# Kernel optimization log

Hardware: AMD Instinct MI355X
Metric: run time of the kernel (lower is better)

## Reference

```python
import jax, jax.numpy as jnp
import numpy as np

TUCKER_RANKS = (8, 2, 6, 2)
N_ITER = 5  # fixed HOOI (ALS) sweeps; tensorly.tucker uses tol-based early stop with n_iter_max=100


def _unfold(t, n):
    return jnp.moveaxis(t, n, 0).reshape(t.shape[n], -1)


def _top_left_vecs(X, r):
    # top-r left singular vectors of X, via eigh on the smaller Gram matrix
    d, k = X.shape
    if d <= k:
        _, v = jnp.linalg.eigh(X @ X.T)  # ascending eigvals
        return v[:, ::-1][:, :r]
    w, v = jnp.linalg.eigh(X.T @ X)
    w = w[::-1][:r]
    v = v[:, ::-1][:, :r]
    return (X @ v) / jnp.sqrt(jnp.maximum(w, 1e-12))


def _mode_dot_t(t, U, mode):
    # tensor x_mode U^T : contracts dim `mode` (size d) down to U.shape[1] (rank r)
    return jnp.moveaxis(jnp.tensordot(t, U, axes=([mode], [0])), -1, mode)


def _project(t, factors, skip):
    # contract modes with the biggest reduction first so intermediates stay tiny
    order = sorted((m for m in range(t.ndim) if m != skip),
                   key=lambda m: factors[m].shape[1] / t.shape[m])
    y = t
    for m in order:
        y = _mode_dot_t(y, factors[m], m)
    return y


def _tucker(t, ranks, n_iter):
    # HOSVD init + HOOI (ALS) sweeps, as in tensorly.decomposition.tucker
    factors = [_top_left_vecs(_unfold(t, n), r) for n, r in enumerate(ranks)]
    for _ in range(n_iter):
        for n in range(len(ranks)):
            y = _project(t, factors, skip=n)
            factors[n] = _top_left_vecs(_unfold(y, n), ranks[n])
    core = _project(t, factors, skip=-1)
    return core, factors


def _forward(state, action, conv_w, conv_b, wa, ba, wq, bq):
    sv = jax.lax.conv_general_dilated(
        state[None], conv_w, window_strides=(1, 1, 1), padding='VALID',
        dimension_numbers=('NCDHW', 'OIDHW', 'NCDHW'))[0]
    sv = jax.nn.relu(sv + conv_b[:, None, None, None])   # [32, 96, 384, 24]
    core, _ = _tucker(sv, TUCKER_RANKS, N_ITER)           # [8, 2, 6, 2]
    av = jax.nn.relu(action @ wa.T + ba)                  # [192]
    sav = jax.nn.relu(core.reshape(-1) + av)              # [192]
    return sav @ wq.T + bq                                # [1]


def setup_inputs() -> dict:
    key = jax.random.key(0)
    ks = jax.random.split(key, 8)
    n_actions = 96
    core_dim = 8 * 2 * 6 * 2  # 192
    return {
        'state': jax.random.normal(ks[0], (4, 96, 386, 24), dtype=jnp.float32),
        'action': jax.random.uniform(ks[1], (n_actions,), dtype=jnp.float32),
        'conv_w': jax.random.normal(ks[2], (32, 4, 1, 3, 1), dtype=jnp.float32) * 0.1,
        'conv_b': jax.random.normal(ks[3], (32,), dtype=jnp.float32) * 0.1,
        'wa': jax.random.normal(ks[4], (core_dim, n_actions), dtype=jnp.float32) * 0.1,
        'ba': jax.random.normal(ks[5], (core_dim,), dtype=jnp.float32) * 0.1,
        'wq': jax.random.normal(ks[6], (1, core_dim), dtype=jnp.float32) * 0.1,
        'bq': jax.random.normal(ks[7], (1,), dtype=jnp.float32) * 0.1,
    }


def reference(state, action, conv_w, conv_b, wa, ba, wq, bq):
    return _forward(state, action, conv_w, conv_b, wa, ba, wq, bq)
```

## Files before the change

kernel.cpp:

```cpp
#include <hip/hip_runtime.h>
#include <math.h>

#define TPB 256
#define SMLSIZ 25
#define D_EPS    1.1102230246251565e-16
#define D_SAFMIN 2.2250738585072014e-308
#define CMDMAX 8192
#define SCHUNK 64

__device__ __forceinline__ double d_sign(double a, double b){
  double aa = fabs(a);
  return (b >= 0.0) ? aa : -aa;
}
__device__ __forceinline__ double dlapy2(double x, double y){
  double xa = fabs(x), ya = fabs(y);
  double w = fmax(xa, ya), z = fmin(xa, ya);
  if (z == 0.0) return w;
  double t = z / w;
  return w * sqrt(1.0 + t*t);
}
__device__ void dlartg(double f, double g, double* cs, double* sn, double* r){
  if (g == 0.0) { *cs = 1.0; *sn = 0.0; *r = f; return; }
  if (f == 0.0) { *cs = 0.0; *sn = (g >= 0.0) ? 1.0 : -1.0; *r = fabs(g); return; }
  double f1 = fabs(f), g1 = fabs(g);
  double rtmin = sqrt(D_SAFMIN);
  double rtmax = sqrt(1.0/(2.0*D_SAFMIN));
  if (f1 > rtmin && f1 < rtmax && g1 > rtmin && g1 < rtmax) {
    double d = sqrt(f*f + g*g);
    *cs = f1 / d;
    double rr = (f >= 0.0) ? d : -d;
    *sn = g / rr;
    *r = rr;
  } else {
    double safmax = 1.0/D_SAFMIN;
    double u = fmin(safmax, fmax(fmax(D_SAFMIN, f1), g1));
    double fs = f/u, gs = g/u;
    double d = sqrt(fs*fs + gs*gs);
    *cs = fabs(fs)/d;
    double rr = (f >= 0.0) ? d : -d;
    *sn = gs / rr;
    *r = rr * u;
  }
}
__device__ void dlaev2(double a, double b, double c,
                       double* rt1, double* rt2, double* cs1, double* sn1){
  double sm = a + c, df = a - c, adf = fabs(df), tb = b + b, ab = fabs(tb);
  double acmx, acmn;
  if (fabs(a) > fabs(c)) { acmx = a; acmn = c; } else { acmx = c; acmn = a; }
  double rt;
  if (adf > ab)      { double t = ab/adf; rt = adf*sqrt(1.0+t*t); }
  else if (adf < ab) { double t = adf/ab; rt = ab*sqrt(1.0+t*t); }
  else               rt = ab*sqrt(2.0);
  int sgn1;
  if (sm < 0.0)      { *rt1 = 0.5*(sm-rt); sgn1 = -1; *rt2 = (acmx / *rt1)*acmn - (b / *rt1)*b; }
  else if (sm > 0.0) { *rt1 = 0.5*(sm+rt); sgn1 =  1; *rt2 = (acmx / *rt1)*acmn - (b / *rt1)*b; }
  else               { *rt1 = 0.5*rt; *rt2 = -0.5*rt; sgn1 = 1; }
  int sgn2; double cs;
  if (df >= 0.0) { cs = df + rt; sgn2 = 1; } else { cs = df - rt; sgn2 = -1; }
  double acs = fabs(cs);
  if (acs > ab) {
    double ct = -tb/cs;
    *sn1 = 1.0/sqrt(1.0+ct*ct);
    *cs1 = ct * (*sn1);
  } else {
    if (ab == 0.0) { *cs1 = 1.0; *sn1 = 0.0; }
    else { double tn = -cs/tb; *cs1 = 1.0/sqrt(1.0+tn*tn); *sn1 = tn * (*cs1); }
  }
  if (sgn1 == sgn2) { double tn = *cs1; *cs1 = -(*sn1); *sn1 = tn; }
}
__device__ void dlamrg(int n1, int n2, const double* a, int s1, int s2, int* idx){
  int n1sv = n1, n2sv = n2;
  int ind1 = (s1 > 0) ? 0 : n1-1;
  int ind2 = (s2 > 0) ? n1 : n1+n2-1;
  int i = 0;
  while (n1sv > 0 && n2sv > 0) {
    if (a[ind1] <= a[ind2]) { idx[i++] = ind1; ind1 += s1; n1sv--; }
    else                    { idx[i++] = ind2; ind2 += s2; n2sv--; }
  }
  while (n1sv > 0) { idx[i++] = ind1; ind1 += s1; n1sv--; }
  while (n2sv > 0) { idx[i++] = ind2; ind2 += s2; n2sv--; }
}

__device__ void my_laed5(int i, const double* d, const double* z, double rho,
                         double* delta, double* lam){
  double del = d[1]-d[0];
  if (i == 0) {
    double w = 1.0 + 2.0*rho*(z[1]*z[1]-z[0]*z[0])/del;
    if (w > 0.0) {
      double b = del + rho*(z[0]*z[0]+z[1]*z[1]);
      double c = rho*z[0]*z[0]*del;
      double tau = 2.0*c/(b+sqrt(fabs(b*b-4.0*c)));
      *lam = d[0] + tau;
      delta[0] = -z[0]/tau;
      delta[1] =  z[1]/(del-tau);
    } else {
      double b = -del + rho*(z[0]*z[0]+z[1]*z[1]);
      double c = rho*z[1]*z[1]*del;
      double tau;
      if (b > 0.0) tau = -2.0*c/(b+sqrt(b*b+4.0*c));
      else         tau = (b - sqrt(b*b+4.0*c))/2.0;
      *lam = d[1] + tau;
      delta[0] = -z[0]/(del+tau);
      delta[1] = -z[1]/tau;
    }
    double temp = dlapy2(delta[0], delta[1]);
    delta[0] /= temp; delta[1] /= temp;
  } else {
    double b = -del + rho*(z[0]*z[0]+z[1]*z[1]);
    double c = rho*z[1]*z[1]*del;
    double tau;
    if (b > 0.0) tau = (b+sqrt(b*b+4.0*c))/2.0;
    else         tau = 2.0*c/(-b+sqrt(b*b+4.0*c));
    *lam = d[1] + tau;
    delta[0] = -z[0]/(del+tau);
    delta[1] = -z[1]/tau;
    double temp = dlapy2(delta[0], delta[1]);
    delta[0] /= temp; delta[1] /= temp;
  }
}
__device__ void my_laed4(int k, int j, const double* dl, const double* w, double rho,
                         double* delta, double* lam){
  if (k == 1) { *lam = dl[0] + rho*w[0]*w[0]; delta[0] = 1.0; return; }
  if (k == 2) { my_laed5(j, dl, w, rho, delta, lam); return; }
  int base; double a, b;
  if (j < k-1) {
    double dj = dl[j], dj1 = dl[j+1];
    double mid = 0.5*(dj+dj1);
    double fm = 1.0;
#pragma unroll 4
    for (int i = 0; i < k; i++) fm += rho*w[i]*w[i]/(dl[i]-mid);
    if (fm >= 0.0) { base = j;   a = 0.0;      b = mid - dj;  }
    else           { base = j+1; a = mid - dj1; b = 0.0;      }
  } else {
    base = k-1;
    double zz = 0.0;
#pragma unroll 4
    for (int i = 0; i < k; i++) zz += w[i]*w[i];
    a = 0.0; b = rho*zz;
    for (int t = 0; t < 64; t++) {
      double g = 1.0;
#pragma unroll 4
      for (int i = 0; i < k; i++) g += rho*w[i]*w[i]/((dl[i]-dl[base]) - b);
      if (g >= 0.0) break;
      b *= 2.0;
    }
  }
  for (int it = 0; it < 140; it++) {
    double m = 0.5*(a+b);
    if (m == a || m == b) break;
    double g = 1.0;
#pragma unroll 4
    for (int i = 0; i < k; i++) g += rho*w[i]*w[i]/((dl[i]-dl[base]) - m);
    if (g >= 0.0) b = m; else a = m;
  }
  double tau = 0.5*(a+b);
  *lam = dl[base] + tau;
#pragma unroll 4
  for (int i = 0; i < k; i++) delta[i] = (dl[i]-dl[base]) - tau;
}

struct Cmd { double c, s; int a, b; };
// ... 590 lines not shown
            }
            __syncthreads();
            if (K == 2) {
              if (tid == 0) {
                for (int j = 0; j < 2; j++) {
                  double a0 = qb[(size_t)j*ldn + 0], a1 = qb[(size_t)j*ldn + 1];
                  qb[(size_t)j*ldn + 0] = (indxc[0] == 0) ? a0 : a1;
                  qb[(size_t)j*ldn + 1] = (indxc[1] == 0) ? a0 : a1;
                }
              }
              __syncthreads();
            } else if (K >= 3) {
              for (int i = tid; i < K; i += NT) szv[i] = sw[i];
              __syncthreads();
              for (int i = tid; i < K; i += NT) {
                double prod = qb[(size_t)i*ldn + i];
#pragma unroll 4
                for (int j = 0; j < K; j++) {
                  if (j == i) continue;
                  prod *= qb[(size_t)j*ldn + i] / (sdl[i]-sdl[j]);
                }
                sw[i] = d_sign(sqrt(fmax(-prod, 0.0)), szv[i]);
              }
              __syncthreads();
              for (int j = tid; j < K; j += NT) {
                double nrm = 0.0;
#pragma unroll 4
                for (int i = 0; i < K; i++) {
                  double v = sw[i]/qb[(size_t)j*ldn + i];
                  sbuf[(size_t)j*K + i] = v;
                  nrm += v*v;
                }
                ss2[j] = sqrt(nrm);
              }
              __syncthreads();
              for (int fl = tid; fl < K*K; fl += NT) {
                int jj2 = fl/K, i = fl%K;
                qb[(size_t)jj2*ldn + i] = sbuf[(size_t)jj2*K + indxc[i]] / ss2[jj2];
              }
              __syncthreads();
            }
            int n12 = ct0+ct1, n23 = ct1+ct2;
            for (int fl = tid; fl < n23*K; fl += NT) {
              int jj2 = fl/n23, i = fl%n23;
              sbuf[(size_t)jj2*n23 + i] = qb[(size_t)jj2*ldn + ct0 + i];
            }
            __syncthreads();
            for (int fl = tid; fl < n2c*K; fl += NT) {
              int jj2 = fl/n2c, r = fl%n2c;
              const double* srow = sbuf + (size_t)jj2*n23;
              double acc = 0.0;
              int l = 0;
              int rem = n23 & 7;
              for (; l < rem; l++) acc += q2[base2 + (size_t)l*n2c + r] * srow[l];
              for (; l < n23; l += 8) {
                double x0 = q2[base2 + (size_t)(l+0)*n2c + r];
                double x1 = q2[base2 + (size_t)(l+1)*n2c + r];
                double x2 = q2[base2 + (size_t)(l+2)*n2c + r];
                double x3 = q2[base2 + (size_t)(l+3)*n2c + r];
                double x4 = q2[base2 + (size_t)(l+4)*n2c + r];
                double x5 = q2[base2 + (size_t)(l+5)*n2c + r];
                double x6 = q2[base2 + (size_t)(l+6)*n2c + r];
                double x7 = q2[base2 + (size_t)(l+7)*n2c + r];
                double y0 = srow[l+0], y1 = srow[l+1], y2 = srow[l+2], y3 = srow[l+3];
                double y4 = srow[l+4], y5 = srow[l+5], y6 = srow[l+6], y7 = srow[l+7];
                acc += x0*y0; acc += x1*y1; acc += x2*y2; acc += x3*y3;
                acc += x4*y4; acc += x5*y5; acc += x6*y6; acc += x7*y7;
              }
              qb[(size_t)jj2*ldn + n1 + r] = acc;
            }
            __syncthreads();
            for (int fl = tid; fl < n12*K; fl += NT) {
              int jj2 = fl/n12, i = fl%n12;
              sbuf[(size_t)jj2*n12 + i] = qb[(size_t)jj2*ldn + i];
            }
            __syncthreads();
            for (int fl = tid; fl < n1*K; fl += NT) {
              int jj2 = fl/n1, r = fl%n1;
              const double* srow = sbuf + (size_t)jj2*n12;
              double acc = 0.0;
              int l = 0;
              int rem = n12 & 7;
              for (; l < rem; l++) acc += q2[(size_t)l*n1 + r] * srow[l];
              for (; l < n12; l += 8) {
                double x0 = q2[(size_t)(l+0)*n1 + r];
                double x1 = q2[(size_t)(l+1)*n1 + r];
                double x2 = q2[(size_t)(l+2)*n1 + r];
                double x3 = q2[(size_t)(l+3)*n1 + r];
                double x4 = q2[(size_t)(l+4)*n1 + r];
                double x5 = q2[(size_t)(l+5)*n1 + r];
                double x6 = q2[(size_t)(l+6)*n1 + r];
                double x7 = q2[(size_t)(l+7)*n1 + r];
                double y0 = srow[l+0], y1 = srow[l+1], y2 = srow[l+2], y3 = srow[l+3];
                double y4 = srow[l+4], y5 = srow[l+5], y6 = srow[l+6], y7 = srow[l+7];
                acc += x0*y0; acc += x1*y1; acc += x2*y2; acc += x3*y3;
                acc += x4*y4; acc += x5*y5; acc += x6*y6; acc += x7*y7;
              }
              qb[(size_t)jj2*ldn + r] = acc;
            }
            __syncthreads();
            if (tid == 0) dlamrg(K, nm-K, dm, 1, -1, ixq);
            __syncthreads();
          }
        }
        if (tid == 0) iw[i2/2] = iw[i2+1];
        __syncthreads();
      }
      sp /= 2;
    }
    {
      int msz2 = finish - startb + 1;
      for (int i = tid; i < msz2; i += NT) dtmp[i] = sd[startb + indxq[startb+i]];
      for (int fl = tid; fl < msz2*msz2; fl += NT) {
        int i = fl/msz2, r = fl%msz2;
        qtmp[(size_t)i*msz2 + r] = Z[(size_t)(startb + indxq[startb+i])*n + startb + r];
      }
      __syncthreads();
      for (int i = tid; i < msz2; i += NT) sd[startb+i] = dtmp[i];
      for (int fl = tid; fl < msz2*msz2; fl += NT) {
        int i = fl/msz2, r = fl%msz2;
        Z[(size_t)(startb+i)*n + startb + r] = qtmp[(size_t)i*msz2 + r];
      }
      __syncthreads();
      if (tid == 0) {
        double onrm = dcom[7];
        for (int i = startb; i <= finish; i++) sd[i] *= onrm;
      }
      __syncthreads();
    }
    startb = finish + 1;
  }
  if (nblk > 1) {
    for (int ii = 1; ii <= n-1; ii++) {
      if (tid == 0) {
        int i = ii-1, kk = i; double p = sd[i];
        for (int j = ii; j <= n-1; j++) if (sd[j] < p) { kk = j; p = sd[j]; }
        icom[7] = kk;
        if (kk != i) { sd[kk] = sd[i]; sd[i] = p; }
      }
      __syncthreads();
      int kk = icom[7], i = ii-1;
      if (kk != i) {
        for (int r = tid; r < n; r += NT) {
          double t = Z[(size_t)i*n + r];
          Z[(size_t)i*n + r] = Z[(size_t)kk*n + r];
          Z[(size_t)kk*n + r] = t;
        }
      }
      __syncthreads();
    }
  }
}

template<int NT, int MAXN>
__global__ __launch_bounds__(NT) void k_eigh_small(int n, const double* __restrict__ Ain,
                                                   double* __restrict__ Zout,
                                                   double* __restrict__ Dout,
                                                   double* gwrk){
  __shared__ double sd[MAXN], se[MAXN], stau[MAXN], sdl[MAXN], sw[MAXN], szv[MAXN], ss2[MAXN];
  __shared__ double red[NT], dcom[8];
  __shared__ int indx[MAXN], indxc[MAXN], indxp[MAXN], coltyp[MAXN], indxq[MAXN];
  __shared__ int iw[40], icom[16], icom2[16];
  __shared__ Cmd scmd[SCHUNK];
  extern __shared__ double dyn[];
  double* A = dyn;
  double* Z = dyn + n*n;
  const int tid = threadIdx.x;

  for (int x = tid; x < n*n; x += NT) A[x] = Ain[x];
  __syncthreads();

  sytd2_dev<NT>(n, A, sd, se, stau, szv, red, dcom);

  for (int x = tid; x < n*n; x += NT) Z[x] = ((x % (n+1)) == 0) ? 1.0 : 0.0;
  __syncthreads();

  stedc_dev<NT>(n, Z, gwrk, sd, se, sdl, sw, szv, ss2, dcom,
                indx, indxc, indxp, coltyp, indxq, iw, icom, icom2, scmd);

  __syncthreads();
  for (int j = tid; j < n; j += NT) {
    for (int ii = n-2; ii >= 0; ii--) {
      double tau_i = stau[ii];
      if (tau_i == 0.0) continue;
      double w = Z[(size_t)j*n + ii + 1];
#pragma unroll 4
      for (int r = ii+2; r < n; r++) w += A[(size_t)ii*n + r] * Z[(size_t)j*n + r];
      w *= tau_i;
      Z[(size_t)j*n + ii + 1] -= w;
#pragma unroll 4
      for (int r = ii+2; r < n; r++) Z[(size_t)j*n + r] -= w * A[(size_t)ii*n + r];
    }
  }
  __syncthreads();
  for (int x = tid; x < n*n; x += NT) Zout[x] = Z[x];
  for (int i = tid; i < n; i += NT) Dout[i] = sd[i];
}

template<int NT>
__global__ __launch_bounds__(NT) void k_sytd2_big(int n, double* A,
                                                  double* gsd, double* gse, double* gtau){
  __shared__ double sd[384], se[384], stau[384], vv[384], ww[384];
  __shared__ double red[16], dcom[8];
  const int tid = threadIdx.x;
  sytd2_big<NT>(n, A, sd, se, stau, vv, ww, red, dcom);
  for (int i = tid; i < n; i += NT) {
    gsd[i] = sd[i];
    gtau[i] = stau[i];
    if (i < n-1) gse[i] = se[i];
  }
}

template<int NT>
__global__ __launch_bounds__(NT) void k_stedc_big(int n, double* Z, double* Dout,
                                                  double* gwrk,
                                                  const double* gsd, const double* gse){
  __shared__ double sd[384], se[384], sdl[384], sw[384], szv[384], ss2[384];
  __shared__ double dcom[8];
  __shared__ int indx[384], indxc[384], indxp[384], coltyp[384], indxq[384];
  __shared__ int iw[40], icom[16], icom2[16];
  __shared__ Cmd scmd[SCHUNK];
  const int tid = threadIdx.x;

  for (int i = tid; i < n; i += NT) {
    sd[i] = gsd[i];
    if (i < n-1) se[i] = gse[i];
  }
  for (size_t x = tid; x < (size_t)n*n; x += NT) Z[x] = ((x % (size_t)(n+1)) == 0) ? 1.0 : 0.0;
  __syncthreads();

  stedc_dev<NT>(n, Z, gwrk, sd, se, sdl, sw, szv, ss2, dcom,
                indx, indxc, indxp, coltyp, indxq, iw, icom, icom2, scmd);

  for (int i = tid; i < n; i += NT) Dout[i] = sd[i];
}

#define OB_COLS 8
__global__ __launch_bounds__(256) void k_ormtr_big(int n, const double* __restrict__ A,
                                                   double* __restrict__ Z,
                                                   const double* __restrict__ tau,
                                                   int col0base){
  __shared__ double zc[OB_COLS][384];
  __shared__ double vsh[384];
  int col0 = col0base + blockIdx.x * OB_COLS;
  int tid = threadIdx.x;
  int c = tid >> 5;
  int l = tid & 31;
  for (int x = tid; x < OB_COLS*n; x += 256) {
    int cc = x / n, r = x % n;
    if (col0+cc < n) zc[cc][r] = Z[(size_t)(col0+cc)*n + r];
  }
  __syncthreads();
  for (int ii = n-2; ii >= 0; ii--) {
    double ti = tau[ii];
    if (ti != 0.0) {
      for (int r = ii+2+tid; r < n; r += 256) vsh[r] = A[(size_t)ii*n + r];
      __syncthreads();
      double p = (l == 0) ? zc[c][ii+1] : 0.0;
#pragma unroll 4
      for (int r = ii+2+l; r < n; r += 32) p += vsh[r]*zc[c][r];
      for (int off = 16; off > 0; off >>= 1) p += __shfl_down(p, off, 32);
      double w = __shfl(p, 0, 32) * ti;
      if (l == 0) zc[c][ii+1] -= w;
#pragma unroll 4
      for (int r = ii+2+l; r < n; r += 32) zc[c][r] -= w*vsh[r];
      __syncthreads();
    }
  }
  for (int x = tid; x < OB_COLS*n; x += 256) {
    int cc = x / n, r = x % n;
    if (col0+cc < n) Z[(size_t)(col0+cc)*n + r] = zc[cc][r];
  }
}

__global__ __launch_bounds__(TPB) void k_conv(const float* __restrict__ st,
                                              const float* __restrict__ cw,
                                              const float* __restrict__ cb,
                                              float* __restrict__ sv){
  int idx = blockIdx.x*TPB + threadIdx.x;
  if (idx >= 28311552) return;
  int w = idx % 24; int t = idx/24;
  int h = t % 384; t /= 384;
  int d = t % 96; int o = t/96;
  float acc = cb[o];
  for (int i = 0; i < 4; i++)
    for (int kh = 0; kh < 3; kh++)
      acc += st[(((size_t)i*96+d)*386 + h+kh)*24 + w] * cw[(o*4+i)*3 + kh];
  sv[idx] = fmaxf(acc, 0.0f);
}

__global__ __launch_bounds__(TPB) void k_g0p(const float* __restrict__ sv, double* parts){
  __shared__ float slab[32*25];
  int b = blockIdx.x;
  double acc[4]; int c1s[4], c2s[4];
#pragma unroll
  for (int k = 0; k < 4; k++) { int e = threadIdx.x + k*TPB; acc[k] = 0.0; c1s[k] = e/32; c2s[k] = e%32; }
  for (int q = 0; q < 128; q++) {
    int s = b*128 + q; int d = s/384, p = s%384;
    for (int l = threadIdx.x; l < 768; l += TPB) {
      int cc = l/24, w = l-cc*24;
      slab[cc*25+w] = sv[(((size_t)cc*96+d)*384+p)*24 + w];
    }
    __syncthreads();
#pragma unroll
    for (int k = 0; k < 4; k++) {
      double sacc = 0.0;
      const float* r1 = slab + c1s[k]*25;
      const float* r2 = slab + c2s[k]*25;
      for (int w = 0; w < 24; w++) sacc += (double)r1[w]*(double)r2[w];
      acc[k] += sacc;
    }
    __syncthreads();
  }
  for (int k = 0; k < 4; k++) parts[(size_t)b*1024 + threadIdx.x + k*TPB] = acc[k];
}
__global__ __launch_bounds__(TPB) void k_g1p(const float* __restrict__ sv, double* parts){
  __shared__ float slab[96*25];
  int c = blockIdx.x;
  double acc[36]; int d1s[36], d2s[36];
#pragma unroll
  for (int k = 0; k < 36; k++) { int e = threadIdx.x + k*TPB; acc[k] = 0.0; d1s[k] = e/96; d2s[k] = e%96; }
  for (int p = 0; p < 384; p++) {
    for (int l = threadIdx.x; l < 2304; l += TPB) {
      int d = l/24, w = l-d*24;
      slab[d*25+w] = sv[(((size_t)c*96+d)*384+p)*24 + w];
    }
    __syncthreads();
#pragma unroll
    for (int k = 0; k < 36; k++) {
      double sacc = 0.0;
      const float* r1 = slab + d1s[k]*25;
      const float* r2 = slab + d2s[k]*25;
      for (int w = 0; w < 24; w++) sacc += (double)r1[w]*(double)r2[w];
      acc[k] += sacc;
    }
    __syncthreads();
  }
  for (int k = 0; k < 36; k++) parts[(size_t)c*9216 + threadIdx.x + k*TPB] = acc[k];
}
#define G2_NKG 6
__global__ __launch_bounds__(TPB) void k_g2p(const float* __restrict__ sv, double* parts){
  __shared__ float aS[64*25], bS[64*25];
  int blk = blockIdx.x;
  int kg = blk/36, t2 = blk%36, tI = t2/6, tJ = t2%6;
  int tr = (threadIdx.x/16)*4, tc = (threadIdx.x%16)*4;
  double acc[4][4];
#pragma unroll
  for (int i = 0; i < 4; i++)
#pragma unroll
    for (int j = 0; j < 4; j++) acc[i][j] = 0.0;
  for (int ss = 0; ss < 512; ss++) {
    int s = kg*512 + ss;
    size_t base = (size_t)s*9216;
    for (int l = threadIdx.x; l < 1536; l += TPB) {
      int row = l/24, w = l-row*24;
      aS[row*25+w] = sv[base + (size_t)tI*1536 + l];
      bS[row*25+w] = sv[base + (size_t)tJ*1536 + l];
    }
    __syncthreads();
    for (int w = 0; w < 24; w++) {
      double a0 = aS[(tr+0)*25+w], a1 = aS[(tr+1)*25+w], a2 = aS[(tr+2)*25+w], a3 = aS[(tr+3)*25+w];
      double b0 = bS[(tc+0)*25+w], b1 = bS[(tc+1)*25+w], b2 = bS[(tc+2)*25+w], b3 = bS[(tc+3)*25+w];
      acc[0][0]+=a0*b0; acc[0][1]+=a0*b1; acc[0][2]+=a0*b2; acc[0][3]+=a0*b3;
      acc[1][0]+=a1*b0; acc[1][1]+=a1*b1; acc[1][2]+=a1*b2; acc[1][3]+=a1*b3;
      acc[2][0]+=a2*b0; acc[2][1]+=a2*b1; acc[2][2]+=a2*b2; acc[2][3]+=a2*b3;
      acc[3][0]+=a3*b0; acc[3][1]+=a3*b1; acc[3][2]+=a3*b2; acc[3][3]+=a3*b3;
    }
    __syncthreads();
  }
  for (int i = 0; i < 4; i++)
    for (int j = 0; j < 4; j++)
      parts[(size_t)kg*147456 + (size_t)(tI*64+tr+i)*384 + (tJ*64+tc+j)] = acc[i][j];
}
__global__ __launch_bounds__(TPB) void k_g3p(const float* __restrict__ sv, double* parts){
  __shared__ float slab[9216];
  int b = blockIdx.x;
  double acc[3]; int w1s[3], w2s[3];
#pragma unroll
  for (int k = 0; k < 3; k++) { int e = threadIdx.x + k*TPB; acc[k] = 0.0; w1s[k] = e/24; w2s[k] = e%24; }
  for (int q = 0; q < 24; q++) {
    int s = b*24 + q;
    size_t base = (size_t)s*9216;
    for (int l = threadIdx.x; l < 9216; l += TPB) slab[l] = sv[base + l];
    __syncthreads();
#pragma unroll
    for (int k = 0; k < 3; k++) {
      int e = threadIdx.x + k*TPB;
// ... 66 lines not shown
    long t = idx;
    int i3 = (int)(t % os3); t /= os3;
    int i2 = (int)(t % os2); t /= os2;
    int i1 = (int)(t % os1); int i0 = (int)(t/os1);
    int j;
    long base; long st; int sa;
    if (ax == 0)      { j = i0; base = (long)i1*str1 + i2*str2 + i3; st = str0; sa = s0; }
    else if (ax == 1) { j = i1; base = (long)i0*str0 + i2*str2 + i3; st = str1; sa = s1; }
    else if (ax == 2) { j = i2; base = (long)i0*str0 + i1*str1 + i3; st = str2; sa = s2; }
    else              { j = i3; base = (long)i0*str0 + i1*str1 + i2*str2; st = str3; sa = s3; }
    double acc = 0.0;
#pragma unroll 4
    for (int c = 0; c < sa; c++) acc += in[base + (long)c*st] * U[c*r + j];
    out[idx] = acc;
  }
}

__global__ __launch_bounds__(TPB) void k_gram_sw0(const double* __restrict__ y, double* G){
  for (int e = threadIdx.x; e < 576; e += TPB) {
    int c1 = e/24, c2 = e%24;
    double acc = 0.0;
#pragma unroll 4
    for (int i = 0; i < 32; i++) acc += y[i*24+c1]*y[i*24+c2];
    G[e] = acc;
  }
}
__global__ __launch_bounds__(TPB) void k_gram_sw1(const double* __restrict__ y, double* G){
  for (int e = threadIdx.x; e < 9216; e += TPB) {
    int d1 = e/96, d2 = e%96;
    double acc = 0.0;
#pragma unroll 2
    for (int a = 0; a < 8; a++)
#pragma unroll
      for (int ee = 0; ee < 6; ee++)
#pragma unroll
        for (int m = 0; m < 2; m++)
          acc += y[(((size_t)a*96+d1)*6+ee)*2+m]*y[(((size_t)a*96+d2)*6+ee)*2+m];
    G[e] = acc;
  }
}
__global__ __launch_bounds__(TPB) void k_gram_sw2(const double* __restrict__ y, double* G){
  for (int e = threadIdx.x; e < 1024; e += TPB) {
    int q1 = e/32, q2 = e%32;
    double acc = 0.0;
#pragma unroll 4
    for (int p = 0; p < 384; p++)
      acc += y[(size_t)(q1>>1)*768 + p*2 + (q1&1)]*y[(size_t)(q2>>1)*768 + p*2 + (q2&1)];
    G[e] = acc;
  }
}
__global__ __launch_bounds__(TPB) void k_gram_sw3(const double* __restrict__ y, double* G){
  for (int e = threadIdx.x; e < 576; e += TPB) {
    int w1 = e/24, w2 = e%24;
    double acc = 0.0;
#pragma unroll 2
    for (int a = 0; a < 8; a++)
#pragma unroll
      for (int j = 0; j < 2; j++)
#pragma unroll
        for (int ee = 0; ee < 6; ee++)
          acc += y[(((size_t)a*2+j)*6+ee)*24+w1]*y[(((size_t)a*2+j)*6+ee)*24+w2];
    G[e] = acc;
  }
}

__global__ __launch_bounds__(TPB) void k_fact_sq(double* U, const double* Z, int n, int r){
  int t = blockIdx.x*TPB + threadIdx.x;
  if (t >= n*r) return;
  int i = t/r, j = t%r;
  U[t] = Z[(size_t)(n-1-j)*n + i];
}
__global__ __launch_bounds__(TPB) void k_factT0(double* U0, const double* y,
                                                const double* Z, const double* D){
  int t = threadIdx.x;
  if (t >= 256) return;
  int i = t/8, j = t%8;
  int col = 23-j;
  double acc = 0.0;
#pragma unroll 4
  for (int c = 0; c < 24; c++) acc += y[i*24+c]*Z[(size_t)col*24+c];
  U0[t] = acc / sqrt(fmax(D[col], 1e-12));
}
__global__ __launch_bounds__(TPB) void k_factT2(double* U2, const double* y,
                                                const double* Z, const double* D){
  int t = blockIdx.x*TPB + threadIdx.x;
  if (t >= 2304) return;
  int p = t/6, j = t%6;
  int col = 31-j;
  double acc = 0.0;
#pragma unroll 4
  for (int q = 0; q < 32; q++)
    acc += y[(size_t)(q>>1)*768 + p*2 + (q&1)]*Z[(size_t)col*32+q];
  U2[t] = acc / sqrt(fmax(D[col], 1e-12));
}

__global__ __launch_bounds__(TPB) void k_tail(const double* __restrict__ core,
                                              const float* __restrict__ action,
                                              const float* __restrict__ wa,
                                              const float* __restrict__ ba,
                                              const float* __restrict__ wq,
                                              const float* __restrict__ bq,
                                              float* __restrict__ out){
  __shared__ double s[TPB];
  int t = threadIdx.x;
  double v = 0.0;
  if (t < 192) {
    double av = 0.0;
#pragma unroll 4
    for (int i = 0; i < 96; i++) av += (double)action[i]*(double)wa[t*96+i];
    av += (double)ba[t];
    if (av < 0.0) av = 0.0;
    double sav = core[t] + av;
    if (sav < 0.0) sav = 0.0;
    v = sav * (double)wq[t];
  }
  s[t] = v; __syncthreads();
  for (int st = 128; st > 0; st >>= 1) { if (t < st) s[t] += s[t+st]; __syncthreads(); }
  if (t == 0) out[0] = (float)(s[0] + (double)bq[0]);
}
__global__ void k_fail(float* out){ out[0] = 1234.5f; }

extern "C" void kernel_launch(void* const* d_in, const int* in_sizes, int n_in,
                              void* d_out, int out_size, void* d_ws, size_t ws_size,
                              hipStream_t stream){
  (void)in_sizes; (void)n_in; (void)out_size;
  const float* state  = (const float*)d_in[0];
  const float* action = (const float*)d_in[1];
  const float* conv_w = (const float*)d_in[2];
  const float* conv_b = (const float*)d_in[3];
  const float* wa     = (const float*)d_in[4];
  const float* ba     = (const float*)d_in[5];
  const float* wq     = (const float*)d_in[6];
  const float* bq     = (const float*)d_in[7];
  float* outp = (float*)d_out;

  char* ws = (char*)d_ws;
  size_t off = 0;
  auto alloc = [&](size_t bytes){ size_t o = off; off = (off + bytes + 255) & ~(size_t)255; return o; };
  size_t o_sv   = alloc(28311552ull*4);
  size_t o_A    = alloc(589824ull*8);
  size_t o_B    = alloc(49152ull*8);
  size_t o_C    = alloc(12288ull*8);
  size_t o_U0   = alloc(32*8*8);
  size_t o_U1   = alloc(96*2*8);
  size_t o_U2   = alloc(384*6*8);
  size_t o_U3   = alloc(24*2*8);
  size_t o_core = alloc(192*8);
  size_t o_G    = alloc(384ull*384*8);
  size_t o_Z    = alloc(384ull*384*8);
  size_t o_D    = alloc(384*8);
  size_t o_Tau  = alloc(384*8);
  size_t o_Sd   = alloc(384*8);
  size_t o_Se   = alloc(384*8);
  size_t o_pts  = alloc(7864320ull);
  if (off > ws_size) { hipLaunchKernelGGL(k_fail, dim3(1), dim3(1), 0, stream, outp); return; }

  float*  sv   = (float*)(ws + o_sv);
  double* bufA = (double*)(ws + o_A);
  double* bufB = (double*)(ws + o_B);
  double* bufC = (double*)(ws + o_C);
  double* U0   = (double*)(ws + o_U0);
  double* U1   = (double*)(ws + o_U1);
  double* U2   = (double*)(ws + o_U2);
  double* U3   = (double*)(ws + o_U3);
  double* core = (double*)(ws + o_core);
  double* G    = (double*)(ws + o_G);
  double* Zb   = (double*)(ws + o_Z);
  double* Db   = (double*)(ws + o_D);
  double* gTau = (double*)(ws + o_Tau);
  double* gSd  = (double*)(ws + o_Sd);
  double* gSe  = (double*)(ws + o_Se);
  double* parts = (double*)(ws + o_pts);
  double* gwrk  = parts;

  auto eigh = [&](int n){
    if (n <= 96) {
      size_t shb = (size_t)2*n*n*8;
      hipLaunchKernelGGL((k_eigh_small<TPB,96>), dim3(1), dim3(TPB), shb, stream,
                         n, G, Zb, Db, gwrk);
    } else {
      hipLaunchKernelGGL((k_sytd2_big<384>), dim3(1), dim3(384), 0, stream,
                         n, G, gSd, gSe, gTau);
      hipLaunchKernelGGL((k_stedc_big<1024>), dim3(1), dim3(1024), 0, stream,
                         n, Zb, Db, gwrk, gSd, gSe);
      hipLaunchKernelGGL(k_ormtr_big, dim3(1), dim3(256), 0, stream,
                         n, G, Zb, gTau, n - OB_COLS);
    }
  };

  hipLaunchKernelGGL(k_conv, dim3(110592), dim3(TPB), 0, stream, state, conv_w, conv_b, sv);

  hipLaunchKernelGGL(k_g0p, dim3(288), dim3(TPB), 0, stream, sv, parts);
  hipLaunchKernelGGL(k_reduce, dim3(4), dim3(TPB), 0, stream, G, parts, 288, 1024);
  eigh(32);
  hipLaunchKernelGGL(k_fact_sq, dim3(1), dim3(TPB), 0, stream, U0, Zb, 32, 8);

  hipLaunchKernelGGL(k_g1p, dim3(32), dim3(TPB), 0, stream, sv, parts);
  hipLaunchKernelGGL(k_reduce, dim3(36), dim3(TPB), 0, stream, G, parts, 32, 9216);
  eigh(96);
  hipLaunchKernelGGL(k_fact_sq, dim3(1), dim3(TPB), 0, stream, U1, Zb, 96, 2);

  hipLaunchKernelGGL(k_g2p, dim3(G2_NKG*36), dim3(TPB), 0, stream, sv, parts);
  hipLaunchKernelGGL(k_reduce, dim3(576), dim3(TPB), 0, stream, G, parts, G2_NKG, 147456);
  eigh(384);
  hipLaunchKernelGGL(k_fact_sq, dim3(9), dim3(TPB), 0, stream, U2, Zb, 384, 6);

  hipLaunchKernelGGL(k_g3p, dim3(128), dim3(TPB), 0, stream, sv, parts);
  hipLaunchKernelGGL(k_reduce, dim3(3), dim3(TPB), 0, stream, G, parts, 128, 576);
  eigh(24);
  hipLaunchKernelGGL(k_fact_sq, dim3(1), dim3(TPB), 0, stream, U3, Zb, 24, 2);

  for (int s = 0; s < 5; s++) {
    hipLaunchKernelGGL(k_c2sv, dim3(3072), dim3(TPB), 0, stream, sv, U2, bufA);
    hipLaunchKernelGGL(k_contract4, dim3(36), dim3(TPB), 0, stream, bufA, U1, bufB, 32,96,6,24, 1, 2);
    hipLaunchKernelGGL(k_contract4, dim3(3),  dim3(TPB), 0, stream, bufB, U3, bufC, 32,2,6,24, 3, 2);
    hipLaunchKernelGGL(k_gram_sw0, dim3(1), dim3(TPB), 0, stream, bufC, G);
    eigh(24);
    hipLaunchKernelGGL(k_factT0, dim3(1), dim3(TPB), 0, stream, U0, bufC, Zb, Db);
    hipLaunchKernelGGL(k_c2sv, dim3(3072), dim3(TPB), 0, stream, sv, U2, bufA);
    hipLaunchKernelGGL(k_contract4, dim3(144), dim3(TPB), 0, stream, bufA, U3, bufB, 32,96,6,24, 3, 2);
    hipLaunchKernelGGL(k_contract4, dim3(36),  dim3(TPB), 0, stream, bufB, U0, bufC, 32,96,6,2, 0, 8);
    hipLaunchKernelGGL(k_gram_sw1, dim3(1), dim3(TPB), 0, stream, bufC, G);
    eigh(96);
    hipLaunchKernelGGL(k_fact_sq, dim3(1), dim3(TPB), 0, stream, U1, Zb, 96, 2);
    hipLaunchKernelGGL(k_c1sv, dim3(1152), dim3(TPB), 0, stream, sv, U1, bufA);
    hipLaunchKernelGGL(k_contract4, dim3(192), dim3(TPB), 0, stream, bufA, U3, bufB, 32,2,384,24, 3, 2);
    hipLaunchKernelGGL(k_contract4, dim3(48),  dim3(TPB), 0, stream, bufB, U0, bufC, 32,2,384,2, 0, 8);
    hipLaunchKernelGGL(k_gram_sw2, dim3(1), dim3(TPB), 0, stream, bufC, G);
    eigh(32);
    hipLaunchKernelGGL(k_factT2, dim3(9), dim3(TPB), 0, stream, U2, bufC, Zb, Db);
    hipLaunchKernelGGL(k_c2sv, dim3(3072), dim3(TPB), 0, stream, sv, U2, bufA);
    hipLaunchKernelGGL(k_contract4, dim3(36), dim3(TPB), 0, stream, bufA, U1, bufB, 32,96,6,24, 1, 2);
    hipLaunchKernelGGL(k_contract4, dim3(9),  dim3(TPB), 0, stream, bufB, U0, bufC, 32,2,6,24, 0, 8);
    hipLaunchKernelGGL(k_gram_sw3, dim3(1), dim3(TPB), 0, stream, bufC, G);
    eigh(24);
    hipLaunchKernelGGL(k_fact_sq, dim3(1), dim3(TPB), 0, stream, U3, Zb, 24, 2);
  }

  hipLaunchKernelGGL(k_c2sv, dim3(3072), dim3(TPB), 0, stream, sv, U2, bufA);
  hipLaunchKernelGGL(k_contract4, dim3(36), dim3(TPB), 0, stream, bufA, U1, bufB, 32,96,6,24, 1, 2);
  hipLaunchKernelGGL(k_contract4, dim3(3),  dim3(TPB), 0, stream, bufB, U3, bufC, 32,2,6,24, 3, 2);
  hipLaunchKernelGGL(k_contract4, dim3(1),  dim3(TPB), 0, stream, bufC, U0, core, 32,2,6,2, 0, 8);

  hipLaunchKernelGGL(k_tail, dim3(1), dim3(TPB), 0, stream, core, action, wa, ba, wq, bq, outp);
}
```

Before: 76.30 ms.

## Parallelize divide-and-conquer merges across blocks and reuse U2-projected buffers

The single-block divide-and-conquer eigensolver for the 384-size eigenproblem is split into a pre-pass, one multi-block launch per merge level where independent merges run in separate blocks, and a final permutation/sort pass. The aim is to spread the serial merge work over several compute units instead of one block. Separately, redundant k_c2sv and contract recomputations are dropped, reusing bufA/bufB from the previous step since U2/U1 have not changed in between. This adds launches and caps the rotation and task buffers (MERGE_CMD, MAXTASK, MLEV), which could overflow or drop merges on other inputs.

```diff
diff --git a/kernel.cpp b/kernel.cpp
--- a/kernel.cpp
+++ b/kernel.cpp
@@ -7,6 +7,11 @@
 #define D_SAFMIN 2.2250738585072014e-308
 #define CMDMAX 8192
 #define SCHUNK 64
+#define MLEV 4
+#define MAXTASK 16
+#define MERGE_CMD 512
+#define GWRK_DBL 983040
+#define CMDTOP_DBL (GWRK_DBL - MAXTASK*MERGE_CMD*3)
 
 __device__ __forceinline__ double d_sign(double a, double b){
   double aa = fabs(a);
@@ -903,6 +908,481 @@
   }
 }
 
+struct MTask { int startb, submat, matsiz, msd2, scrOff, cmdSlot; };
+struct Sched {
+  int mcount[MLEV];
+  MTask mt[MLEV][MAXTASK];
+  int npb; int pad;
+  int pb_start[64]; int pb_msz[64]; int pb_isDC[64];
+  double pb_onrm[64];
+};
+
+template<int NT>
+__global__ __launch_bounds__(NT) void k_stedc_pre(int n, double* Z, double* gwrk,
+                                                  double* gSd, double* gSe, int* gIxq,
+                                                  Sched* sc){
+  __shared__ double sd[384], se[384];
+  __shared__ int ixq[384];
+  __shared__ int iw[40], icom[16], icom2[16];
+  __shared__ Cmd scmd[SCHUNK];
+  const int tid = threadIdx.x;
+  for (int i = tid; i < n; i += NT){ sd[i] = gSd[i]; ixq[i] = 0; }
+  for (int i = tid; i < n-1; i += NT) se[i] = gSe[i];
+  for (size_t x = tid; x < (size_t)n*n; x += NT) Z[x] = ((x % (size_t)(n+1)) == 0) ? 1.0 : 0.0;
+  if (tid == 0){ for (int L = 0; L < MLEV; L++) sc->mcount[L] = 0; sc->npb = 0; }
+  __syncthreads();
+  long offL[MLEV] = {0,0,0,0};
+  int startb = 0;
+  while (startb < n) {
+    if (tid == 0) {
+      int finish = startb;
+      while (finish < n-1) {
+        double tiny = D_EPS*sqrt(fabs(sd[finish]))*sqrt(fabs(sd[finish+1]));
+        if (fabs(se[finish]) > tiny) finish++; else break;
+      }
+      icom[9] = finish;
+      int p = sc->npb;
+      int msz = finish - startb + 1;
+      sc->pb_start[p] = startb; sc->pb_msz[p] = msz;
+      sc->pb_isDC[p] = (msz > SMLSIZ) ? 1 : 0;
+      sc->pb_onrm[p] = 1.0;
+      sc->npb = p+1;
+    }
+    __syncthreads();
+    int finish = icom[9];
+    int msz = finish - startb + 1;
+    if (msz == 1) { startb = finish+1; __syncthreads(); continue; }
+    if (msz <= SMLSIZ) {
+      dev_steqr<NT>(msz, sd+startb, se+startb, Z + (size_t)startb*n + startb, n,
+                    (Cmd*)gwrk, icom, scmd);
+      startb = finish+1; __syncthreads(); continue;
+    }
+    if (tid == 0) {
+      double onrm = 0.0;
+      for (int i = startb; i <= finish; i++) onrm = fmax(onrm, fabs(sd[i]));
+      for (int i = startb; i <  finish; i++) onrm = fmax(onrm, fabs(se[i]));
+      if (onrm == 0.0) onrm = 1.0;
+      sc->pb_onrm[sc->npb - 1] = onrm;
+      double inv = 1.0/onrm;
+      for (int i = startb; i <= finish; i++) sd[i] *= inv;
+      for (int i = startb; i <  finish; i++) se[i] *= inv;
+      iw[0] = msz; int sp0 = 1;
+      while (iw[sp0-1] > SMLSIZ) {
+        for (int j = sp0-1; j >= 0; j--) { iw[2*j+1] = (iw[j]+1)/2; iw[2*j] = iw[j]/2; }
+        sp0 *= 2;
+      }
+      for (int j = 1; j < sp0; j++) iw[j] += iw[j-1];
+      icom[8] = sp0;
+      for (int i = 0; i < sp0-1; i++) {
+        int bb = startb + iw[i] - 1;
+        sd[bb]   -= fabs(se[bb]);
+        sd[bb+1] -= fabs(se[bb]);
+      }
+    }
+    __syncthreads();
+    int sp = icom[8];
+    {
+      const int wid = tid >> 6, lane = tid & 63;
+      const int nwaves = NT/64;
+      Cmd* cb0 = (Cmd*)gwrk;
+      for (int li = wid; li < sp; li += nwaves) {
+        if (lane == 0) {
+          int submat = (li == 0) ? 0 : iw[li-1];
+          int matsiz = iw[li] - submat;
+          icom2[li] = (matsiz > 1)
+            ? steqr_scan(matsiz, sd+startb+submat, se+startb+submat, cb0 + (size_t)li*CMDMAX, CMDMAX)
+            : 0;
+        }
+      }
+      __syncthreads();
+      for (int li = wid; li < sp; li += nwaves) {
+        int submat = (li == 0) ? 0 : iw[li-1];
+        int matsiz = iw[li] - submat;
+        int nc = icom2[li];
+        double* zb = Z + (size_t)(startb+submat)*n + (startb+submat);
+        Cmd* cb = cb0 + (size_t)li*CMDMAX;
+        if (lane < matsiz) {
+#pragma unroll 2
+          for (int q = 0; q < nc; q++) apply_cmd(cb[q], zb, n, lane);
+        }
+      }
+      __syncthreads();
+      for (int x = tid; x < msz; x += NT) {
+        int sub = 0;
+        for (int t = 0; t < sp; t++) { if (x < iw[t]) { sub = (t == 0) ? 0 : iw[t-1]; break; } }
+        ixq[startb + x] = x - sub;
+      }
+      __syncthreads();
+    }
+    if (tid == 0) {
+      int lvl = 0, spp = sp;
+      while (spp > 1 && lvl < MLEV) {
+        for (int i2 = 0; i2 <= spp-2; i2 += 2) {
+          int submat, matsiz, msd2;
+          if (i2 == 0) { submat = 0; matsiz = iw[1]; msd2 = iw[0]; }
+          else { submat = iw[i2-1]; matsiz = iw[i2+1]-iw[i2-1]; msd2 = matsiz/2; }
+          int slot = sc->mcount[lvl];
+          if (slot < MAXTASK) {
+            MTask tk; tk.startb = startb; tk.submat = submat; tk.matsiz = matsiz;
+            tk.msd2 = msd2; tk.scrOff = (int)offL[lvl]; tk.cmdSlot = slot;
+            sc->mt[lvl][slot] = tk;
+            sc->mcount[lvl] = slot+1;
+            offL[lvl] += 3L*matsiz*matsiz;
+          }
+          iw[i2/2] = iw[i2+1];
+        }
+        spp /= 2; lvl++;
+      }
+    }
+    __syncthreads();
+    startb = finish + 1;
+  }
+  __syncthreads();
+  for (int i = tid; i < n; i += NT) { gSd[i] = sd[i]; gIxq[i] = ixq[i]; }
+  for (int i = tid; i < n-1; i += NT) gSe[i] = se[i];
+}
+
+template<int NT>
+__global__ __launch_bounds__(NT) void k_stedc_merge(int n, int level, double* Z,
+                                                    double* gwrk, double* gSd,
+                                                    const double* gSe, int* gIxq,
+                                                    Sched* sc){
+  __shared__ double dml[384], sdl[384], sw[384], szv[384], ss2[384];
+  __shared__ double dcom[4];
+  __shared__ int ixql[384], indx[384], indxc[384], indxp[384], coltyp[384];
+  __shared__ int icom[8];
+  __shared__ Cmd scmd[SCHUNK];
+  const int tid = threadIdx.x;
+  if ((int)blockIdx.x >= sc->mcount[level]) return;
+  MTask tk = sc->mt[level][blockIdx.x];
+  const int nm = tk.matsiz, n1 = tk.msd2, ldn = n;
+  const int base0 = tk.startb + tk.submat;
+  double* qb = Z + (size_t)base0*n + base0;
+  double* q2 = gwrk + tk.scrOff;
+  double* sbuf = q2 + 2*(size_t)nm*nm;
+  Cmd* cbuf = (Cmd*)(gwrk + CMDTOP_DBL) + (size_t)tk.cmdSlot*MERGE_CMD;
+  double rho_in = gSe[base0 + n1 - 1];
+
+  for (int i = tid; i < nm; i += NT) { dml[i] = gSd[base0+i]; ixql[i] = gIxq[base0+i]; }
+  __syncthreads();
+  for (int i = tid; i < n1; i += NT)      szv[i] = qb[(size_t)i*ldn + (n1-1)];
+  for (int i = n1+tid; i < nm; i += NT)   szv[i] = qb[(size_t)i*ldn + n1];
+  __syncthreads();
+  if (tid == 0) {
+    int nrot = 0;
+    const int n2_ = nm - n1;
+    double rho = rho_in;
+    if (rho < 0.0) for (int i = n1; i < nm; i++) szv[i] = -szv[i];
+    double tsc = 1.0/sqrt(2.0);
+    for (int i = 0; i < nm; i++) szv[i] *= tsc;
+    rho = fabs(2.0*rho);
+    dcom[0] = rho;
+    for (int i = n1; i < nm; i++) ixql[i] += n1;
+    for (int i = 0; i < nm; i++) sdl[i] = dml[ixql[i]];
+    dlamrg(n1, n2_, sdl, 1, 1, indxc);
+    for (int i = 0; i < nm; i++) indx[i] = ixql[indxc[i]];
+    int imax = 0, jmax = 0;
+    for (int i = 1; i < nm; i++) {
+      if (fabs(szv[i]) > fabs(szv[imax])) imax = i;
+      if (fabs(dml[i]) > fabs(dml[jmax])) jmax = i;
+    }
+    double tol = 8.0*D_EPS*fmax(fabs(dml[jmax]), fabs(szv[imax]));
+    if (rho*fabs(szv[imax]) <= tol) {
+      icom[1] = 0;
+      for (int j = 0; j < nm; j++) sdl[j] = dml[indx[j]];
+    } else {
+      for (int i = 0; i < n1; i++) coltyp[i] = 0;
+      for (int i = n1; i < nm; i++) coltyp[i] = 2;
+      int k = 0, k2 = nm;
+      int pj = 0, jj = 0;
+      bool haveP = false;
+      for (jj = 0; jj < nm; jj++) {
+        int nj = indx[jj];
+        if (rho*fabs(szv[nj]) <= tol) { k2--; coltyp[nj] = 3; indxp[k2] = nj; }
+        else { pj = nj; haveP = true; jj++; break; }
+      }
+      if (haveP) {
+        while (1) {
+          if (jj > nm-1) break;
+          int nj = indx[jj];
+          if (rho*fabs(szv[nj]) <= tol) { k2--; coltyp[nj] = 3; indxp[k2] = nj; }
+          else {
+            double s_ = szv[pj], c_ = szv[nj];
+            double tau = dlapy2(c_, s_);
+            double tdf = dml[nj] - dml[pj];
+            c_ = c_/tau; s_ = -s_/tau;
+            if (fabs(tdf*c_*s_) <= tol) {
+              szv[nj] = tau; szv[pj] = 0.0;
+              if (coltyp[nj] != coltyp[pj]) coltyp[nj] = 1;
+              coltyp[pj] = 3;
+              if (nrot < MERGE_CMD) { cbuf[nrot].c = c_; cbuf[nrot].s = s_; cbuf[nrot].a = pj; cbuf[nrot].b = nj; }
+              nrot++;
+              double t2 = dml[pj]*c_*c_ + dml[nj]*s_*s_;
+              dml[nj] = dml[pj]*s_*s_ + dml[nj]*c_*c_;
+              dml[pj] = t2;
+              k2--;
+              int i1 = 1;
+              while (1) {
+                if (k2 + i1 <= nm-1) {
+                  if (dml[pj] < dml[indxp[k2+i1]]) {
+                    indxp[k2+i1-1] = indxp[k2+i1];
+                    indxp[k2+i1] = pj;
+                    i1++;
+                  } else { indxp[k2+i1-1] = pj; break; }
+                } else { indxp[k2+i1-1] = pj; break; }
+              }
+              pj = nj;
+            } else {
+              k++; sdl[k-1] = dml[pj]; sw[k-1] = szv[pj]; indxp[k-1] = pj; pj = nj;
+            }
+          }
+          jj++;
+        }
+        k++; sdl[k-1] = dml[pj]; sw[k-1] = szv[pj]; indxp[k-1] = pj;
+      }
+      int ct[4] = {0,0,0,0};
+      for (int j = 0; j < nm; j++) ct[coltyp[j]]++;
+      int psm[4];
+      psm[0] = 0; psm[1] = ct[0]; psm[2] = ct[0]+ct[1]; psm[3] = ct[0]+ct[1]+ct[2];
+      for (int j = 0; j < nm; j++) {
+        int js = indxp[j], c4 = coltyp[js];
+        indx[psm[c4]] = js; indxc[psm[c4]] = j; psm[c4]++;
+      }
+      icom[1] = k; icom[2] = ct[0]; icom[3] = ct[1]; icom[4] = ct[2]; icom[5] = ct[3];
+    }
+    icom[6] = (nrot <= MERGE_CMD) ? nrot : MERGE_CMD;
+  }
+  __syncthreads();
+  {
+    int nrot = icom[6];
+    for (int base = 0; base < nrot; base += SCHUNK) {
+      int cnt = nrot - base; if (cnt > SCHUNK) cnt = SCHUNK;
+      for (int q = tid; q < cnt; q += NT) scmd[q] = cbuf[base+q];
+      __syncthreads();
+      for (int r = tid; r < nm; r += NT) {
+#pragma unroll 2
+        for (int q = 0; q < cnt; q++) {
+          Cmd cm = scmd[q];
+          double x = qb[(size_t)cm.a*ldn + r], y = qb[(size_t)cm.b*ldn + r];
+          qb[(size_t)cm.a*ldn + r] = cm.c*x + cm.s*y;
+          qb[(size_t)cm.b*ldn + r] = cm.c*y - cm.s*x;
+        }
+      }
+      __syncthreads();
+    }
+  }
+  int K = icom[1];
+  if (K == 0) {
+    for (int fl = tid; fl < nm*nm; fl += NT) {
+      int jj2 = fl/nm, r = fl%nm;
+      q2[(size_t)jj2*nm + r] = qb[(size_t)indx[jj2]*ldn + r];
+    }
+    __syncthreads();
+    for (int fl = tid; fl < nm*nm; fl += NT) {
+      int jj2 = fl/nm, r = fl%nm;
+      qb[(size_t)jj2*ldn + r] = q2[(size_t)jj2*nm + r];
+    }
+    for (int i = tid; i < nm; i += NT) dml[i] = sdl[i];
+    for (int i = tid; i < nm; i += NT) ixql[i] = i;
+    __syncthreads();
+  } else {
+    int ct0 = icom[2], ct1 = icom[3], ct2 = icom[4];
+    int n2c = nm - n1;
+    int base2 = (ct0+ct1)*n1;
+    int base4 = base2 + (ct1+ct2)*n2c;
+    for (int i = tid; i < nm; i += NT) {
+      int js = indx[i];
+      const double* col = qb + (size_t)js*ldn;
+      if (i < ct0) {
+        double* dst = q2 + (size_t)i*n1;
+#pragma unroll 4
+        for (int r = 0; r < n1; r++) dst[r] = col[r];
+      } else if (i < ct0+ct1) {
+        double* d1 = q2 + (size_t)i*n1;
+#pragma unroll 4
+        for (int r = 0; r < n1; r++) d1[r] = col[r];
+        double* d2 = q2 + base2 + (size_t)(i-ct0)*n2c;
+#pragma unroll 4
+        for (int r = 0; r < n2c; r++) d2[r] = col[n1+r];
+      } else if (i < K) {
+        double* d2 = q2 + base2 + (size_t)(i-ct0)*n2c;
+#pragma unroll 4
+        for (int r = 0; r < n2c; r++) d2[r] = col[n1+r];
+      } else {
+        double* d4 = q2 + base4 + (size_t)(i-K)*nm;
+#pragma unroll 4
+        for (int r = 0; r < nm; r++) d4[r] = col[r];
+      }
+      szv[i] = dml[js];
+    }
+    __syncthreads();
+    for (int fl = tid; fl < (nm-K)*nm; fl += NT) {
+      int jj2 = fl/nm, r = fl%nm;
+      qb[(size_t)(K+jj2)*ldn + r] = q2[base4 + (size_t)jj2*nm + r];
+    }
+    for (int i = K+tid; i < nm; i += NT) dml[i] = szv[i];
+    __syncthreads();
+    double rho = dcom[0];
+    for (int j = tid; j < K; j += NT) {
+      double lam;
+      my_laed4(K, j, sdl, sw, rho, qb + (size_t)j*ldn, &lam);
+      dml[j] = lam;
+    }
+    __syncthreads();
+    if (K == 2) {
+      if (tid == 0) {
+        for (int j = 0; j < 2; j++) {
+          double a0 = qb[(size_t)j*ldn + 0], a1 = qb[(size_t)j*ldn + 1];
+          qb[(size_t)j*ldn + 0] = (indxc[0] == 0) ? a0 : a1;
+          qb[(size_t)j*ldn + 1] = (indxc[1] == 0) ? a0 : a1;
+        }
+      }
+      __syncthreads();
+    } else if (K >= 3) {
+      for (int i = tid; i < K; i += NT) szv[i] = sw[i];
+      __syncthreads();
+      for (int i = tid; i < K; i += NT) {
+        double prod = qb[(size_t)i*ldn + i];
+#pragma unroll 4
+        for (int j = 0; j < K; j++) {
+          if (j == i) continue;
+          prod *= qb[(size_t)j*ldn + i] / (sdl[i]-sdl[j]);
+        }
+        sw[i] = d_sign(sqrt(fmax(-prod, 0.0)), szv[i]);
+      }
+      __syncthreads();
+      for (int j = tid; j < K; j += NT) {
+        double nrm = 0.0;
+#pragma unroll 4
+        for (int i = 0; i < K; i++) {
+          double v = sw[i]/qb[(size_t)j*ldn + i];
+          sbuf[(size_t)j*K + i] = v;
+          nrm += v*v;
+        }
+        ss2[j] = sqrt(nrm);
+      }
+      __syncthreads();
+      for (int fl = tid; fl < K*K; fl += NT) {
+        int jj2 = fl/K, i = fl%K;
+        qb[(size_t)jj2*ldn + i] = sbuf[(size_t)jj2*K + indxc[i]] / ss2[jj2];
+      }
+      __syncthreads();
+    }
+    int n12 = ct0+ct1, n23 = ct1+ct2;
+    for (int fl = tid; fl < n23*K; fl += NT) {
+      int jj2 = fl/n23, i = fl%n23;
+      sbuf[(size_t)jj2*n23 + i] = qb[(size_t)jj2*ldn + ct0 + i];
+    }
+    __syncthreads();
+    for (int fl = tid; fl < n2c*K; fl += NT) {
+      int jj2 = fl/n2c, r = fl%n2c;
+      const double* srow = sbuf + (size_t)jj2*n23;
+      double acc = 0.0;
+      int l = 0;
+      int rem = n23 & 7;
+      for (; l < rem; l++) acc += q2[base2 + (size_t)l*n2c + r] * srow[l];
+      for (; l < n23; l += 8) {
+        double x0 = q2[base2 + (size_t)(l+0)*n2c + r];
+        double x1 = q2[base2 + (size_t)(l+1)*n2c + r];
+        double x2 = q2[base2 + (size_t)(l+2)*n2c + r];
+        double x3 = q2[base2 + (size_t)(l+3)*n2c + r];
+        double x4 = q2[base2 + (size_t)(l+4)*n2c + r];
+        double x5 = q2[base2 + (size_t)(l+5)*n2c + r];
+        double x6 = q2[base2 + (size_t)(l+6)*n2c + r];
+        double x7 = q2[base2 + (size_t)(l+7)*n2c + r];
+        double y0 = srow[l+0], y1 = srow[l+1], y2 = srow[l+2], y3 = srow[l+3];
+        double y4 = srow[l+4], y5 = srow[l+5], y6 = srow[l+6], y7 = srow[l+7];
+        acc += x0*y0; acc += x1*y1; acc += x2*y2; acc += x3*y3;
+        acc += x4*y4; acc += x5*y5; acc += x6*y6; acc += x7*y7;
+      }
+      qb[(size_t)jj2*ldn + n1 + r] = acc;
+    }
+    __syncthreads();
+    for (int fl = tid; fl < n12*K; fl += NT) {
+      int jj2 = fl/n12, i = fl%n12;
+      sbuf[(size_t)jj2*n12 + i] = qb[(size_t)jj2*ldn + i];
+    }
+    __syncthreads();
+    for (int fl = tid; fl < n1*K; fl += NT) {
+      int jj2 = fl/n1, r = fl%n1;
+      const double* srow = sbuf + (size_t)jj2*n12;
+      double acc = 0.0;
+      int l = 0;
+      int rem = n12 & 7;
+      for (; l < rem; l++) acc += q2[(size_t)l*n1 + r] * srow[l];
+      for (; l < n12; l += 8) {
+        double x0 = q2[(size_t)(l+0)*n1 + r];
+        double x1 = q2[(size_t)(l+1)*n1 + r];
+        double x2 = q2[(size_t)(l+2)*n1 + r];
+        double x3 = q2[(size_t)(l+3)*n1 + r];
+        double x4 = q2[(size_t)(l+4)*n1 + r];
+        double x5 = q2[(size_t)(l+5)*n1 + r];
+        double x6 = q2[(size_t)(l+6)*n1 + r];
+        double x7 = q2[(size_t)(l+7)*n1 + r];
+        double y0 = srow[l+0], y1 = srow[l+1], y2 = srow[l+2], y3 = srow[l+3];
+        double y4 = srow[l+4], y5 = srow[l+5], y6 = srow[l+6], y7 = srow[l+7];
+        acc += x0*y0; acc += x1*y1; acc += x2*y2; acc += x3*y3;
+        acc += x4*y4; acc += x5*y5; acc += x6*y6; acc += x7*y7;
+      }
+      qb[(size_t)jj2*ldn + r] = acc;
+    }
+    __syncthreads();
+    if (tid == 0) dlamrg(K, nm-K, dml, 1, -1, ixql);
+    __syncthreads();
+  }
+  for (int i = tid; i < nm; i += NT) { gSd[base0+i] = dml[i]; gIxq[base0+i] = ixql[i]; }
+}
+
+template<int NT>
+__global__ __launch_bounds__(NT) void k_stedc_fin(int n, double* Z, double* Dout,
+                                                  double* gwrk, double* gSd, int* gIxq,
+                                                  Sched* sc){
+  __shared__ int icom[4];
+  const int tid = threadIdx.x;
+  double* qtmp = gwrk;
+  double* dtmp = gwrk + (size_t)n*n;
+  int npb = sc->npb;
+  for (int p = 0; p < npb; p++) {
+    int s = sc->pb_start[p], msz = sc->pb_msz[p];
+    if (sc->pb_isDC[p]) {
+      double onrm = sc->pb_onrm[p];
+      for (int i = tid; i < msz; i += NT) dtmp[i] = gSd[s + gIxq[s+i]];
+      for (int fl = tid; fl < msz*msz; fl += NT) {
+        int i = fl/msz, r = fl%msz;
+        qtmp[(size_t)i*msz + r] = Z[(size_t)(s + gIxq[s+i])*n + s + r];
+      }
+      __syncthreads();
+      for (int i = tid; i < msz; i += NT) gSd[s+i] = dtmp[i]*onrm;
+      for (int fl = tid; fl < msz*msz; fl += NT) {
+        int i = fl/msz, r = fl%msz;
+        Z[(size_t)(s+i)*n + s + r] = qtmp[(size_t)i*msz + r];
+      }
+      __syncthreads();
+    }
+  }
+  if (npb > 1) {
+    for (int ii = 1; ii <= n-1; ii++) {
+      if (tid == 0) {
+        int i = ii-1, kk = i; double p = gSd[i];
+        for (int j = ii; j <= n-1; j++) if (gSd[j] < p) { kk = j; p = gSd[j]; }
+        icom[0] = kk;
+        if (kk != i) { gSd[kk] = gSd[i]; gSd[i] = p; }
+      }
+      __syncthreads();
+      int kk = icom[0], i = ii-1;
+      if (kk != i) {
+        for (int r = tid; r < n; r += NT) {
+          double t = Z[(size_t)i*n + r];
+          Z[(size_t)i*n + r] = Z[(size_t)kk*n + r];
+          Z[(size_t)kk*n + r] = t;
+        }
+      }
+      __syncthreads();
+    }
+  }
+  for (int i = tid; i < n; i += NT) Dout[i] = gSd[i];
+}
+
 template<int NT, int MAXN>
 __global__ __launch_bounds__(NT) void k_eigh_small(int n, const double* __restrict__ Ain,
                                                    double* __restrict__ Zout,
@@ -960,30 +1440,6 @@
     gtau[i] = stau[i];
     if (i < n-1) gse[i] = se[i];
   }
-}
-
-template<int NT>
-__global__ __launch_bounds__(NT) void k_stedc_big(int n, double* Z, double* Dout,
-                                                  double* gwrk,
-                                                  const double* gsd, const double* gse){
-  __shared__ double sd[384], se[384], sdl[384], sw[384], szv[384], ss2[384];
-  __shared__ double dcom[8];
-  __shared__ int indx[384], indxc[384], indxp[384], coltyp[384], indxq[384];
-  __shared__ int iw[40], icom[16], icom2[16];
-  __shared__ Cmd scmd[SCHUNK];
-  const int tid = threadIdx.x;
-
-  for (int i = tid; i < n; i += NT) {
-    sd[i] = gsd[i];
-    if (i < n-1) se[i] = gse[i];
-  }
-  for (size_t x = tid; x < (size_t)n*n; x += NT) Z[x] = ((x % (size_t)(n+1)) == 0) ? 1.0 : 0.0;
-  __syncthreads();
-
-  stedc_dev<NT>(n, Z, gwrk, sd, se, sdl, sw, szv, ss2, dcom,
-                indx, indxc, indxp, coltyp, indxq, iw, icom, icom2, scmd);
-
-  for (int i = tid; i < n; i += NT) Dout[i] = sd[i];
 }
 
 #define OB_COLS 8
@@ -1356,6 +1812,8 @@
   size_t o_Tau  = alloc(384*8);
   size_t o_Sd   = alloc(384*8);
   size_t o_Se   = alloc(384*8);
+  size_t o_Ixq  = alloc(384*4);
+  size_t o_schd = alloc(8192);
   size_t o_pts  = alloc(7864320ull);
   if (off > ws_size) { hipLaunchKernelGGL(k_fail, dim3(1), dim3(1), 0, stream, outp); return; }
 
@@ -1374,6 +1832,8 @@
   double* gTau = (double*)(ws + o_Tau);
   double* gSd  = (double*)(ws + o_Sd);
   double* gSe  = (double*)(ws + o_Se);
+  int*    gIxq = (int*)(ws + o_Ixq);
+  Sched*  schd = (Sched*)(ws + o_schd);
   double* parts = (double*)(ws + o_pts);
   double* gwrk  = parts;
 
@@ -1385,8 +1845,13 @@
     } else {
       hipLaunchKernelGGL((k_sytd2_big<384>), dim3(1), dim3(384), 0, stream,
                          n, G, gSd, gSe, gTau);
-      hipLaunchKernelGGL((k_stedc_big<1024>), dim3(1), dim3(1024), 0, stream,
-                         n, Zb, Db, gwrk, gSd, gSe);
+      hipLaunchKernelGGL((k_stedc_pre<1024>), dim3(1), dim3(1024), 0, stream,
+                         n, Zb, gwrk, gSd, gSe, gIxq, schd);
+      for (int L = 0; L < MLEV; L++)
+        hipLaunchKernelGGL((k_stedc_merge<512>), dim3(MAXTASK), dim3(512), 0, stream,
+                           n, L, Zb, gwrk, gSd, gSe, gIxq, schd);
+      hipLaunchKernelGGL((k_stedc_fin<1024>), dim3(1), dim3(1024), 0, stream,
+                         n, Zb, Db, gwrk, gSd, gIxq, schd);
       hipLaunchKernelGGL(k_ormtr_big, dim3(1), dim3(256), 0, stream,
                          n, G, Zb, gTau, n - OB_COLS);
     }
@@ -1421,7 +1886,6 @@
     hipLaunchKernelGGL(k_gram_sw0, dim3(1), dim3(TPB), 0, stream, bufC, G);
     eigh(24);
     hipLaunchKernelGGL(k_factT0, dim3(1), dim3(TPB), 0, stream, U0, bufC, Zb, Db);
-    hipLaunchKernelGGL(k_c2sv, dim3(3072), dim3(TPB), 0, stream, sv, U2, bufA);
     hipLaunchKernelGGL(k_contract4, dim3(144), dim3(TPB), 0, stream, bufA, U3, bufB, 32,96,6,24, 3, 2);
     hipLaunchKernelGGL(k_contract4, dim3(36),  dim3(TPB), 0, stream, bufB, U0, bufC, 32,96,6,2, 0, 8);
     hipLaunchKernelGGL(k_gram_sw1, dim3(1), dim3(TPB), 0, stream, bufC, G);
@@ -1441,8 +1905,6 @@
     hipLaunchKernelGGL(k_fact_sq, dim3(1), dim3(TPB), 0, stream, U3, Zb, 24, 2);
   }
 
-  hipLaunchKernelGGL(k_c2sv, dim3(3072), dim3(TPB), 0, stream, sv, U2, bufA);
-  hipLaunchKernelGGL(k_contract4, dim3(36), dim3(TPB), 0, stream, bufA, U1, bufB, 32,96,6,24, 1, 2);
   hipLaunchKernelGGL(k_contract4, dim3(3),  dim3(TPB), 0, stream, bufB, U3, bufC, 32,2,6,24, 3, 2);
   hipLaunchKernelGGL(k_contract4, dim3(1),  dim3(TPB), 0, stream, bufC, U0, core, 32,2,6,2, 0, 8);
 
```

Result: faster. 69.53 ms (-8.9%).
